# Kernel optimization log

Measured on AMD Instinct MI355X. Metric: run time of the kernel, lower is better.

The kernel has to match this reference:

```python
import math
import jax, jax.numpy as jnp
import numpy as np

SQRT_2_OVER_PI = 0.7978845608028654
FACIL_RATE = 2.0
FIRE_THRESH = 0.88
EPS = 1e-05

def _gelu(x):
    return 0.5 * x * (1.0 + jnp.tanh(SQRT_2_OVER_PI * (x + 0.044715 * x ** 3)))

def setup_inputs() -> dict:
    key = jax.random.key(0)
    ks = jax.random.split(key, 8)
    B, T, D, N = 4, 4096, 1024, 512
    x = jax.random.normal(ks[0], (B, T, D), jnp.float32)
    ema_x = jax.random.normal(ks[1], (D,), jnp.float32) * 0.1
    ema_x2 = ema_x ** 2 + jax.random.uniform(ks[2], (D,), jnp.float32) + 0.5
    ema_y = jax.random.normal(ks[3], (D,), jnp.float32) * 0.1
    ema_y2 = ema_y ** 2 + jax.random.uniform(ks[4], (D,), jnp.float32) + 0.5
    buf = jax.random.normal(ks[5], (N, D), jnp.float32)
    buf = buf / jnp.linalg.norm(buf, axis=-1, keepdims=True)
    facil = 1.0 + 2.0 * jax.random.uniform(ks[6], (N,), jnp.float32)  # facilitation levels >= 1
    mask = jnp.ones((N,), dtype=bool)
    return {
        'x': x,
        'log_tau_in': jnp.float32(math.log(1.0)),
        'log_tau_out': jnp.float32(math.log(1.0)),
        'log_a_in': jnp.float32(0.0),
        'log_a_out': jnp.float32(0.0),
        'log_k_boost': jnp.float32(math.log(0.5)),
        'log_k_damp': jnp.float32(math.log(0.3)),
        'ema_x': ema_x, 'ema_x2': ema_x2, 'ema_y': ema_y, 'ema_y2': ema_y2,
        'buf': buf, 'facil': facil, 'mask': mask,
    }

def reference(x, log_tau_in, log_tau_out, log_a_in, log_a_out,
              log_k_boost, log_k_damp, ema_x, ema_x2, ema_y, ema_y2,
              buf, facil, mask):
    sg = jax.lax.stop_gradient
    D = x.shape[-1]
    y = _gelu(x)
    # --- gate_211 (l1_ready steady state); z-statistics are detached in torch ---
    tau_in, tau_out = jnp.exp(log_tau_in), jnp.exp(log_tau_out)
    a_in, a_out = jax.nn.sigmoid(log_a_in), jax.nn.sigmoid(log_a_out)
    std_x = jnp.sqrt(jnp.clip(sg(ema_x2) - sg(ema_x) ** 2, 0.0)) + EPS
    z_in = jnp.mean(((sg(x) - sg(ema_x)) / std_x) ** 2, axis=-1)        # [B,T]
    std_y = jnp.sqrt(jnp.clip(sg(ema_y2) - sg(ema_y) ** 2, 0.0)) + EPS
    z_out = jnp.mean(((sg(y) - sg(ema_y)) / std_y) ** 2, axis=-1)       # [B,T]
    g_in = 1.0 - a_in + a_in * jnp.exp(-tau_in * z_in)
    g_out = 1.0 - a_out + a_out * jnp.exp(-tau_out * z_out)
    gate = g_in * g_out
    y1 = y * gate[..., None]
    # --- eval-time OCS nearest-neighbor facilitation (l2_ready, pass1_complete) ---
    k_boost = jnp.clip(jnp.exp(log_k_boost), 0.01, 4.0)
    k_damp = jnp.clip(jnp.exp(log_k_damp), 0.01, 0.9)
    y1_mean = jnp.mean(sg(y1).reshape(-1, D), axis=0)                    # [D]
    m_n = y1_mean / jnp.maximum(jnp.linalg.norm(y1_mean), 1e-12)
    buf_sg = sg(buf)
    buf_n = buf_sg / jnp.maximum(jnp.linalg.norm(buf_sg, axis=-1, keepdims=True), 1e-12)
    sims = jnp.where(mask, buf_n @ m_n, -1.0)                            # [N]
    nearest_idx = jnp.argmax(sims)
    sim_val = jnp.clip(sims[nearest_idx], 0.0, 1.0)
    fired = sim_val > FIRE_THRESH
    facil_level = sg(facil)[nearest_idx] * jnp.where(fired, FACIL_RATE, 1.0)
    v = buf_sg[nearest_idx]                                              # [D]
    valid = jnp.all(jnp.isfinite(v)) & (jnp.linalg.norm(v) >= 1e-06)
    mod = (facil_level - 1.0) * sim_val
    boost = 1.0 + sg(k_boost) * mod            # torch uses .item(): detached
    damp = jnp.maximum(0.01, 1.0 - sg(k_damp) * mod)
    proj = jnp.sum(y1 * v, axis=-1, keepdims=True)
    y_par = proj * v
    out = jnp.where(valid, y_par * boost + (y1 - y_par) * damp, y1)
    return out
```

## Files before the change

kernel.cpp:

```cpp
#include <hip/hip_runtime.h>
#include <math.h>

#define D 1024
#define NROWS 16384
#define NBUF 512

#define OFF_MEAN 0
#define OFF_KEY  1024
#define OFF_RES  1026
#define OFF_GATE 1032
#define ZERO_BYTES 4112

typedef float nfloat4 __attribute__((ext_vector_type(4)));

__device__ __forceinline__ float4 ld4(const float* p) { return *(const float4*)p; }
__device__ __forceinline__ void st4_nt(float* p, float4 v) {
    nfloat4 nv = { v.x, v.y, v.z, v.w };
    __builtin_nontemporal_store(nv, (nfloat4*)p);
}

__device__ __forceinline__ float wave_red(float v) {
    #pragma unroll
    for (int off = 32; off > 0; off >>= 1) v += __shfl_xor(v, off, 64);
    return v;
}

__device__ __forceinline__ float gelu_f(float x) {
    float u = 0.7978845608028654f * (x + 0.044715f * x * x * x);
    float e = __expf(2.0f * u);
    float t = 1.0f - 2.0f / (e + 1.0f);
    return 0.5f * x * (1.0f + t);
}

__device__ __forceinline__ float4 inv_std4(float4 m, float4 m2) {
    float4 r;
    r.x = 1.0f / (sqrtf(fmaxf(m2.x - m.x * m.x, 0.f)) + 1e-5f);
    r.y = 1.0f / (sqrtf(fmaxf(m2.y - m.y * m.y, 0.f)) + 1e-5f);
    r.z = 1.0f / (sqrtf(fmaxf(m2.z - m.z * m.z, 0.f)) + 1e-5f);
    r.w = 1.0f / (sqrtf(fmaxf(m2.w - m.w * m.w, 0.f)) + 1e-5f);
    return r;
}

__global__ __launch_bounds__(256, 4) void k_passA(const float* __restrict__ x,
                                                  const float* __restrict__ ema_x,
                                                  const float* __restrict__ ema_x2,
                                                  const float* __restrict__ ema_y,
                                                  const float* __restrict__ ema_y2,
                                                  const float* __restrict__ lti,
                                                  const float* __restrict__ lto,
                                                  const float* __restrict__ lai,
                                                  const float* __restrict__ lao,
                                                  float* __restrict__ ws) {
    __shared__ float s_acc[D];
    const int tid = threadIdx.x;
    const int wave = tid >> 6, lane = tid & 63;
    for (int i = tid; i < D; i += 256) s_acc[i] = 0.0f;
    __syncthreads();

    const float tau_in = __expf(lti[0]), tau_out = __expf(lto[0]);
    const float a_in  = 1.0f / (1.0f + __expf(-lai[0]));
    const float a_out = 1.0f / (1.0f + __expf(-lao[0]));

    int col[4];
    float4 emx[4], isx[4], emy[4], isy[4];
    #pragma unroll
    for (int j = 0; j < 4; ++j) {
        col[j] = 4 * lane + 256 * j;
        emx[j] = ld4(&ema_x[col[j]]);
        isx[j] = inv_std4(emx[j], ld4(&ema_x2[col[j]]));
        emy[j] = ld4(&ema_y[col[j]]);
        isy[j] = inv_std4(emy[j], ld4(&ema_y2[col[j]]));
    }
    float4 acc[4];
    #pragma unroll
    for (int j = 0; j < 4; ++j) acc[j] = make_float4(0.f, 0.f, 0.f, 0.f);

    const int r0 = (blockIdx.x * 4 + wave) * 4;
    for (int r = r0; r < r0 + 4; ++r) {
        const float* xr = x + (size_t)r * D;
        float4 yv[4];
        float zin = 0.f, zout = 0.f;
        #pragma unroll
        for (int j = 0; j < 4; ++j) {
            float4 xv = ld4(&xr[col[j]]);
            float dx, dy;
            dx = (xv.x - emx[j].x) * isx[j].x; zin += dx * dx;
            dx = (xv.y - emx[j].y) * isx[j].y; zin += dx * dx;
            dx = (xv.z - emx[j].z) * isx[j].z; zin += dx * dx;
            dx = (xv.w - emx[j].w) * isx[j].w; zin += dx * dx;
            yv[j].x = gelu_f(xv.x); dy = (yv[j].x - emy[j].x) * isy[j].x; zout += dy * dy;
            yv[j].y = gelu_f(xv.y); dy = (yv[j].y - emy[j].y) * isy[j].y; zout += dy * dy;
            yv[j].z = gelu_f(xv.z); dy = (yv[j].z - emy[j].z) * isy[j].z; zout += dy * dy;
            yv[j].w = gelu_f(xv.w); dy = (yv[j].w - emy[j].w) * isy[j].w; zout += dy * dy;
        }
        zin  = wave_red(zin)  * (1.0f / D);
        zout = wave_red(zout) * (1.0f / D);
        float g = ((1.0f - a_in)  + a_in  * __expf(-tau_in  * zin)) *
                  ((1.0f - a_out) + a_out * __expf(-tau_out * zout));
        if (lane == 0) ws[OFF_GATE + r] = g;
        #pragma unroll
        for (int j = 0; j < 4; ++j) {
            acc[j].x += yv[j].x * g;
            acc[j].y += yv[j].y * g;
            acc[j].z += yv[j].z * g;
            acc[j].w += yv[j].w * g;
        }
    }
    #pragma unroll
    for (int j = 0; j < 4; ++j) {
        atomicAdd(&s_acc[col[j] + 0], acc[j].x);
        atomicAdd(&s_acc[col[j] + 1], acc[j].y);
        atomicAdd(&s_acc[col[j] + 2], acc[j].z);
        atomicAdd(&s_acc[col[j] + 3], acc[j].w);
    }
    __syncthreads();
    for (int i = tid; i < D; i += 256) atomicAdd(&ws[OFF_MEAN + i], s_acc[i]);
}

__global__ __launch_bounds__(256) void k_sims(const float* __restrict__ buf,
                                              const unsigned char* __restrict__ mask,
                                              float* __restrict__ ws) {
    __shared__ float s_red[4];
    __shared__ float s_inv;
    const int tid = threadIdx.x, wave = tid >> 6, lane = tid & 63;

    float4 mv = ld4(&ws[OFF_MEAN + tid * 4]);
    float ns = mv.x * mv.x + mv.y * mv.y + mv.z * mv.z + mv.w * mv.w;
    ns = wave_red(ns);
    if (lane == 0) s_red[wave] = ns;
    __syncthreads();
    if (tid == 0) {
        float t = s_red[0] + s_red[1] + s_red[2] + s_red[3];
        s_inv = 1.0f / fmaxf(sqrtf(t), 1e-12f);
    }
    __syncthreads();
    const float inv = s_inv;

    int col[4];
    float4 mvv[4];
    #pragma unroll
    for (int j = 0; j < 4; ++j) {
        col[j] = 4 * lane + 256 * j;
        mvv[j] = ld4(&ws[OFF_MEAN + col[j]]);
    }
    unsigned long long* keyp = (unsigned long long*)&ws[OFF_KEY];
    const int n0 = (blockIdx.x * 4 + wave) * 4;
    for (int n = n0; n < n0 + 4; ++n) {
        const float* br = buf + (size_t)n * D;
        float dot = 0.f, bns = 0.f;
        #pragma unroll
        for (int j = 0; j < 4; ++j) {
            float4 bv = ld4(&br[col[j]]);
            dot += bv.x * mvv[j].x + bv.y * mvv[j].y + bv.z * mvv[j].z + bv.w * mvv[j].w;
            bns += bv.x * bv.x + bv.y * bv.y + bv.z * bv.z + bv.w * bv.w;
        }
        dot = wave_red(dot);
        bns = wave_red(bns);
        if (lane == 0) {
            float sim = -1.0f;
            if (mask[n]) sim = (dot * inv) / fmaxf(sqrtf(bns), 1e-12f);
            unsigned int fb = __float_as_uint(sim);
            unsigned int mono = (fb & 0x80000000u) ? ~fb : (fb | 0x80000000u);
            unsigned long long key = ((unsigned long long)mono << 32) | (unsigned int)(~n);
            atomicMax(keyp, key);
        }
    }
}

__global__ __launch_bounds__(1024) void k_final(const float* __restrict__ buf,
                                                const float* __restrict__ facil,
                                                const float* __restrict__ lkb,
                                                const float* __restrict__ lkd,
                                                float* __restrict__ ws) {
    __shared__ float s_sum[16];
    __shared__ int s_fin;
    const int tid = threadIdx.x, wave = tid >> 6, lane = tid & 63;
    if (tid == 0) s_fin = 1;
    __syncthreads();

    unsigned long long key = *(const unsigned long long*)&ws[OFF_KEY];
    int idx = (int)(~(unsigned int)(key & 0xFFFFFFFFull));
    unsigned int mono = (unsigned int)(key >> 32);
    unsigned int fb = (mono & 0x80000000u) ? (mono ^ 0x80000000u) : ~mono;
    float sim = __uint_as_float(fb);

    float v = buf[(size_t)idx * D + tid];
    if (!isfinite(v)) atomicAnd(&s_fin, 0);
    float ns = wave_red(v * v);
    if (lane == 0) s_sum[wave] = ns;
    __syncthreads();
    if (tid == 0) {
        float t = 0.f;
        #pragma unroll
        for (int i = 0; i < 16; ++i) t += s_sum[i];
        float nrm = sqrtf(t);
        int valid = s_fin && (nrm >= 1e-6f);
        float sim_val = fminf(fmaxf(sim, 0.0f), 1.0f);
        float fl = facil[idx] * ((sim_val > 0.88f) ? 2.0f : 1.0f);
        float mod = (fl - 1.0f) * sim_val;
        float kb = fminf(fmaxf(expf(lkb[0]), 0.01f), 4.0f);
        float kd = fminf(fmaxf(expf(lkd[0]), 0.01f), 0.9f);
        float boost = 1.0f + kb * mod;
        float damp = fmaxf(0.01f, 1.0f - kd * mod);
        int* wi = (int*)ws;
        wi[OFF_RES + 0] = idx;
        wi[OFF_RES + 1] = valid;
        ws[OFF_RES + 2] = boost;
        ws[OFF_RES + 3] = damp;
    }
}

__global__ __launch_bounds__(256, 4) void k_passB(const float* __restrict__ x,
                                                  const float* __restrict__ buf,
                                                  const float* __restrict__ ws,
                                                  float* __restrict__ out) {
    const int tid = threadIdx.x, wave = tid >> 6, lane = tid & 63;
    const int* wi = (const int*)ws;
    const int idx = wi[OFF_RES + 0];
    const int valid = wi[OFF_RES + 1];
    const float boost = ws[OFF_RES + 2], damp = ws[OFF_RES + 3];
    const float dampe = valid ? damp : 1.0f;
    const float coef = valid ? (boost - damp) : 0.0f;

    int col[4];
    float4 vv[4];
    const float* vrow = buf + (size_t)idx * D;
    #pragma unroll
    for (int j = 0; j < 4; ++j) {
        col[j] = 4 * lane + 256 * j;
        vv[j] = ld4(&vrow[col[j]]);
        if (!valid) vv[j] = make_float4(0.f, 0.f, 0.f, 0.f);
    }

    const int r0 = (blockIdx.x * 4 + wave) * 4;
    for (int r = r0; r < r0 + 4; ++r) {
        const float* xr = x + (size_t)r * D;
        const float g = ws[OFF_GATE + r];
        float4 y1[4];
        float proj = 0.f;
        #pragma unroll
        for (int j = 0; j < 4; ++j) {
            float4 xv = ld4(&xr[col[j]]);
            y1[j].x = gelu_f(xv.x) * g; proj += y1[j].x * vv[j].x;
            y1[j].y = gelu_f(xv.y) * g; proj += y1[j].y * vv[j].y;
            y1[j].z = gelu_f(xv.z) * g; proj += y1[j].z * vv[j].z;
            y1[j].w = gelu_f(xv.w) * g; proj += y1[j].w * vv[j].w;
        }
        proj = wave_red(proj);
        const float pc = proj * coef;
        float* orow = out + (size_t)r * D;
        #pragma unroll
        for (int j = 0; j < 4; ++j) {
            float4 o;
            o.x = y1[j].x * dampe + pc * vv[j].x;
            o.y = y1[j].y * dampe + pc * vv[j].y;
            o.z = y1[j].z * dampe + pc * vv[j].z;
            o.w = y1[j].w * dampe + pc * vv[j].w;
            st4_nt(&orow[col[j]], o);
        }
    }
}

extern "C" void kernel_launch(void* const* d_in, const int* in_sizes, int n_in,
                              void* d_out, int out_size, void* d_ws, size_t ws_size,
                              hipStream_t stream) {
    const float* x      = (const float*)d_in[0];
    const float* lti    = (const float*)d_in[1];
    const float* lto    = (const float*)d_in[2];
    const float* lai    = (const float*)d_in[3];
    const float* lao    = (const float*)d_in[4];
    const float* lkb    = (const float*)d_in[5];
    const float* lkd    = (const float*)d_in[6];
    const float* ema_x  = (const float*)d_in[7];
    const float* ema_x2 = (const float*)d_in[8];
    const float* ema_y  = (const float*)d_in[9];
    const float* ema_y2 = (const float*)d_in[10];
    const float* buf    = (const float*)d_in[11];
    const float* facil  = (const float*)d_in[12];
    const unsigned char* mask = (const unsigned char*)d_in[13];
    float* ws  = (float*)d_ws;
    float* out = (float*)d_out;

    (void)hipMemsetAsync(d_ws, 0, ZERO_BYTES, stream);
    hipLaunchKernelGGL(k_passA, dim3(1024), dim3(256), 0, stream,
                       x, ema_x, ema_x2, ema_y, ema_y2, lti, lto, lai, lao, ws);
    hipLaunchKernelGGL(k_sims,  dim3(32),  dim3(256), 0, stream, buf, mask, ws);
    hipLaunchKernelGGL(k_final, dim3(1),   dim3(1024), 0, stream, buf, facil, lkb, lkd, ws);
    hipLaunchKernelGGL(k_passB, dim3(1024), dim3(256), 0, stream, x, buf, ws, out);
}
```

Baseline: 196.6 us.

## Replace global atomics with partial sums, fold final into passB, widen grids

Pass A now writes per-block partial column sums to workspace instead of issuing global atomics. A new small kernel reduces groups of 16 partials before atomically accumulating the mean. The sims kernel uses one row per wave across 128 blocks. The single-block final kernel is removed, and each passB block recomputes boost, damp and validity itself, with passB using 2048 blocks of 2 rows per wave. The aim is to cut atomic contention and launch serialization, at the cost of an extra kernel, redundant per-block scalar work and workspace traffic for the partials.

```diff
diff --git a/kernel.cpp b/kernel.cpp
--- a/kernel.cpp
+++ b/kernel.cpp
@@ -7,8 +7,8 @@
 
 #define OFF_MEAN 0
 #define OFF_KEY  1024
-#define OFF_RES  1026
-#define OFF_GATE 1032
+#define OFF_GATE 2048
+#define OFF_PART 20480
 #define ZERO_BYTES 4112
 
 typedef float nfloat4 __attribute__((ext_vector_type(4)));
@@ -41,6 +41,7 @@
     return r;
 }
 
+template<int RPW>
 __global__ __launch_bounds__(256, 4) void k_passA(const float* __restrict__ x,
                                                   const float* __restrict__ ema_x,
                                                   const float* __restrict__ ema_x2,
@@ -75,8 +76,8 @@
     #pragma unroll
     for (int j = 0; j < 4; ++j) acc[j] = make_float4(0.f, 0.f, 0.f, 0.f);
 
-    const int r0 = (blockIdx.x * 4 + wave) * 4;
-    for (int r = r0; r < r0 + 4; ++r) {
+    const int r0 = (blockIdx.x * 4 + wave) * RPW;
+    for (int r = r0; r < r0 + RPW; ++r) {
         const float* xr = x + (size_t)r * D;
         float4 yv[4];
         float zin = 0.f, zout = 0.f;
@@ -114,7 +115,23 @@
         atomicAdd(&s_acc[col[j] + 3], acc[j].w);
     }
     __syncthreads();
-    for (int i = tid; i < D; i += 256) atomicAdd(&ws[OFF_MEAN + i], s_acc[i]);
+    float4 pv = *(float4*)&s_acc[tid * 4];
+    *(float4*)&ws[OFF_PART + (size_t)blockIdx.x * D + tid * 4] = pv;
+}
+
+__global__ __launch_bounds__(256) void k_mean(float* __restrict__ ws) {
+    const int tid = threadIdx.x;
+    const float* P = &ws[OFF_PART + (size_t)blockIdx.x * 16 * D];
+    float4 s = make_float4(0.f, 0.f, 0.f, 0.f);
+    #pragma unroll
+    for (int i = 0; i < 16; ++i) {
+        float4 v = ld4(&P[(size_t)i * D + 4 * tid]);
+        s.x += v.x; s.y += v.y; s.z += v.z; s.w += v.w;
+    }
+    atomicAdd(&ws[OFF_MEAN + 4 * tid + 0], s.x);
+    atomicAdd(&ws[OFF_MEAN + 4 * tid + 1], s.y);
+    atomicAdd(&ws[OFF_MEAN + 4 * tid + 2], s.z);
+    atomicAdd(&ws[OFF_MEAN + 4 * tid + 3], s.w);
 }
 
 __global__ __launch_bounds__(256) void k_sims(const float* __restrict__ buf,
@@ -143,97 +160,84 @@
         col[j] = 4 * lane + 256 * j;
         mvv[j] = ld4(&ws[OFF_MEAN + col[j]]);
     }
-    unsigned long long* keyp = (unsigned long long*)&ws[OFF_KEY];
-    const int n0 = (blockIdx.x * 4 + wave) * 4;
-    for (int n = n0; n < n0 + 4; ++n) {
-        const float* br = buf + (size_t)n * D;
-        float dot = 0.f, bns = 0.f;
-        #pragma unroll
-        for (int j = 0; j < 4; ++j) {
-            float4 bv = ld4(&br[col[j]]);
-            dot += bv.x * mvv[j].x + bv.y * mvv[j].y + bv.z * mvv[j].z + bv.w * mvv[j].w;
-            bns += bv.x * bv.x + bv.y * bv.y + bv.z * bv.z + bv.w * bv.w;
-        }
-        dot = wave_red(dot);
-        bns = wave_red(bns);
-        if (lane == 0) {
-            float sim = -1.0f;
-            if (mask[n]) sim = (dot * inv) / fmaxf(sqrtf(bns), 1e-12f);
-            unsigned int fb = __float_as_uint(sim);
-            unsigned int mono = (fb & 0x80000000u) ? ~fb : (fb | 0x80000000u);
-            unsigned long long key = ((unsigned long long)mono << 32) | (unsigned int)(~n);
-            atomicMax(keyp, key);
-        }
-    }
-}
-
-__global__ __launch_bounds__(1024) void k_final(const float* __restrict__ buf,
-                                                const float* __restrict__ facil,
-                                                const float* __restrict__ lkb,
-                                                const float* __restrict__ lkd,
-                                                float* __restrict__ ws) {
-    __shared__ float s_sum[16];
-    __shared__ int s_fin;
+    const int n = blockIdx.x * 4 + wave;
+    const float* br = buf + (size_t)n * D;
+    float dot = 0.f, bns = 0.f;
+    #pragma unroll
+    for (int j = 0; j < 4; ++j) {
+        float4 bv = ld4(&br[col[j]]);
+        dot += bv.x * mvv[j].x + bv.y * mvv[j].y + bv.z * mvv[j].z + bv.w * mvv[j].w;
+        bns += bv.x * bv.x + bv.y * bv.y + bv.z * bv.z + bv.w * bv.w;
+    }
+    dot = wave_red(dot);
+    bns = wave_red(bns);
+    if (lane == 0) {
+        float sim = -1.0f;
+        if (mask[n]) sim = (dot * inv) / fmaxf(sqrtf(bns), 1e-12f);
+        unsigned int fb = __float_as_uint(sim);
+        unsigned int mono = (fb & 0x80000000u) ? ~fb : (fb | 0x80000000u);
+        unsigned long long key = ((unsigned long long)mono << 32) | (unsigned int)(~n);
+        atomicMax((unsigned long long*)&ws[OFF_KEY], key);
+    }
+}
+
+__global__ __launch_bounds__(256, 4) void k_passB(const float* __restrict__ x,
+                                                  const float* __restrict__ buf,
+                                                  const float* __restrict__ facil,
+                                                  const float* __restrict__ lkb,
+                                                  const float* __restrict__ lkd,
+                                                  const float* __restrict__ ws,
+                                                  float* __restrict__ out) {
+    __shared__ float s_red[4];
+    __shared__ float s_sc[3];
     const int tid = threadIdx.x, wave = tid >> 6, lane = tid & 63;
-    if (tid == 0) s_fin = 1;
-    __syncthreads();
-
-    unsigned long long key = *(const unsigned long long*)&ws[OFF_KEY];
-    int idx = (int)(~(unsigned int)(key & 0xFFFFFFFFull));
-    unsigned int mono = (unsigned int)(key >> 32);
-    unsigned int fb = (mono & 0x80000000u) ? (mono ^ 0x80000000u) : ~mono;
-    float sim = __uint_as_float(fb);
-
-    float v = buf[(size_t)idx * D + tid];
-    if (!isfinite(v)) atomicAnd(&s_fin, 0);
-    float ns = wave_red(v * v);
-    if (lane == 0) s_sum[wave] = ns;
+
+    const unsigned long long key = *(const unsigned long long*)&ws[OFF_KEY];
+    const int idx = (int)(~(unsigned int)(key & 0xFFFFFFFFull));
+    const unsigned int mono = (unsigned int)(key >> 32);
+    const unsigned int fb = (mono & 0x80000000u) ? (mono ^ 0x80000000u) : ~mono;
+    const float sim = __uint_as_float(fb);
+
+    int col[4];
+    float4 vv[4];
+    const float* vrow = buf + (size_t)idx * D;
+    float bns = 0.f;
+    #pragma unroll
+    for (int j = 0; j < 4; ++j) {
+        col[j] = 4 * lane + 256 * j;
+        vv[j] = ld4(&vrow[col[j]]);
+        if (!isfinite(vv[j].x)) bns = __uint_as_float(0x7FC00000u);
+        if (!isfinite(vv[j].y)) bns = __uint_as_float(0x7FC00000u);
+        if (!isfinite(vv[j].z)) bns = __uint_as_float(0x7FC00000u);
+        if (!isfinite(vv[j].w)) bns = __uint_as_float(0x7FC00000u);
+        bns += vv[j].x * vv[j].x + vv[j].y * vv[j].y + vv[j].z * vv[j].z + vv[j].w * vv[j].w;
+    }
+    bns = wave_red(bns);
+    if (lane == 0) s_red[wave] = bns;
     __syncthreads();
     if (tid == 0) {
-        float t = 0.f;
-        #pragma unroll
-        for (int i = 0; i < 16; ++i) t += s_sum[i];
-        float nrm = sqrtf(t);
-        int valid = s_fin && (nrm >= 1e-6f);
+        float t = s_red[0] + s_red[1] + s_red[2] + s_red[3];
+        int valid = (t >= 1e-12f) ? 1 : 0;
         float sim_val = fminf(fmaxf(sim, 0.0f), 1.0f);
         float fl = facil[idx] * ((sim_val > 0.88f) ? 2.0f : 1.0f);
         float mod = (fl - 1.0f) * sim_val;
-        float kb = fminf(fmaxf(expf(lkb[0]), 0.01f), 4.0f);
-        float kd = fminf(fmaxf(expf(lkd[0]), 0.01f), 0.9f);
+        float kb = fminf(fmaxf(__expf(lkb[0]), 0.01f), 4.0f);
+        float kd = fminf(fmaxf(__expf(lkd[0]), 0.01f), 0.9f);
         float boost = 1.0f + kb * mod;
         float damp = fmaxf(0.01f, 1.0f - kd * mod);
-        int* wi = (int*)ws;
-        wi[OFF_RES + 0] = idx;
-        wi[OFF_RES + 1] = valid;
-        ws[OFF_RES + 2] = boost;
-        ws[OFF_RES + 3] = damp;
-    }
-}
-
-__global__ __launch_bounds__(256, 4) void k_passB(const float* __restrict__ x,
-                                                  const float* __restrict__ buf,
-                                                  const float* __restrict__ ws,
-                                                  float* __restrict__ out) {
-    const int tid = threadIdx.x, wave = tid >> 6, lane = tid & 63;
-    const int* wi = (const int*)ws;
-    const int idx = wi[OFF_RES + 0];
-    const int valid = wi[OFF_RES + 1];
-    const float boost = ws[OFF_RES + 2], damp = ws[OFF_RES + 3];
-    const float dampe = valid ? damp : 1.0f;
-    const float coef = valid ? (boost - damp) : 0.0f;
-
-    int col[4];
-    float4 vv[4];
-    const float* vrow = buf + (size_t)idx * D;
-    #pragma unroll
-    for (int j = 0; j < 4; ++j) {
-        col[j] = 4 * lane + 256 * j;
-        vv[j] = ld4(&vrow[col[j]]);
-        if (!valid) vv[j] = make_float4(0.f, 0.f, 0.f, 0.f);
-    }
-
-    const int r0 = (blockIdx.x * 4 + wave) * 4;
-    for (int r = r0; r < r0 + 4; ++r) {
+        s_sc[0] = valid ? damp : 1.0f;
+        s_sc[1] = valid ? (boost - damp) : 0.0f;
+        s_sc[2] = (float)valid;
+    }
+    __syncthreads();
+    const float dampe = s_sc[0], coef = s_sc[1];
+    if (s_sc[2] == 0.0f) {
+        #pragma unroll
+        for (int j = 0; j < 4; ++j) vv[j] = make_float4(0.f, 0.f, 0.f, 0.f);
+    }
+
+    const int r0 = (blockIdx.x * 4 + wave) * 2;
+    for (int r = r0; r < r0 + 2; ++r) {
         const float* xr = x + (size_t)r * D;
         const float g = ws[OFF_GATE + r];
         float4 y1[4];
@@ -281,10 +285,23 @@
     float* ws  = (float*)d_ws;
     float* out = (float*)d_out;
 
+    int NP;
+    if      (ws_size >= ((size_t)OFF_PART + 2048u * D) * 4) NP = 2048;
+    else if (ws_size >= ((size_t)OFF_PART + 1024u * D) * 4) NP = 1024;
+    else                                                    NP = 512;
+
     (void)hipMemsetAsync(d_ws, 0, ZERO_BYTES, stream);
-    hipLaunchKernelGGL(k_passA, dim3(1024), dim3(256), 0, stream,
-                       x, ema_x, ema_x2, ema_y, ema_y2, lti, lto, lai, lao, ws);
-    hipLaunchKernelGGL(k_sims,  dim3(32),  dim3(256), 0, stream, buf, mask, ws);
-    hipLaunchKernelGGL(k_final, dim3(1),   dim3(1024), 0, stream, buf, facil, lkb, lkd, ws);
-    hipLaunchKernelGGL(k_passB, dim3(1024), dim3(256), 0, stream, x, buf, ws, out);
-}
+    if (NP == 2048)
+        hipLaunchKernelGGL(k_passA<2>, dim3(2048), dim3(256), 0, stream,
+                           x, ema_x, ema_x2, ema_y, ema_y2, lti, lto, lai, lao, ws);
+    else if (NP == 1024)
+        hipLaunchKernelGGL(k_passA<4>, dim3(1024), dim3(256), 0, stream,
+                           x, ema_x, ema_x2, ema_y, ema_y2, lti, lto, lai, lao, ws);
+    else
+        hipLaunchKernelGGL(k_passA<8>, dim3(512), dim3(256), 0, stream,
+                           x, ema_x, ema_x2, ema_y, ema_y2, lti, lto, lai, lao, ws);
+    hipLaunchKernelGGL(k_mean,  dim3(NP / 16), dim3(256), 0, stream, ws);
+    hipLaunchKernelGGL(k_sims,  dim3(128), dim3(256), 0, stream, buf, mask, ws);
+    hipLaunchKernelGGL(k_passB, dim3(2048), dim3(256), 0, stream,
+                       x, buf, facil, lkb, lkd, ws, out);
+}
```

Result: slower. 217.8 us (+10.8%).
